# Optimization experiments

Hardware: AMD Instinct MI355X
Metric: run time of the kernel (lower is better)

Reference implementation:

```python
import jax, jax.numpy as jnp
import numpy as np

B, T, C, H, D = 16, 512, 464, 16, 29  # head_size = n_embd // n_head = 29
EPS = 1e-5


def setup_inputs() -> dict:
    key = jax.random.key(0)
    ks = jax.random.split(key, 8)
    x = jax.random.normal(ks[0], (B, T, C), dtype=jnp.float32)
    # relative-position indices: idx[i, j] = clip(i - j, 0, T-1)
    i = jnp.arange(T)
    pos_idx = jnp.clip(i[:, None] - i[None, :], 0, T - 1).astype(jnp.int64)
    s = 0.02
    wq = jax.random.normal(ks[1], (H, C, D), dtype=jnp.float32) * s
    wk = jax.random.normal(ks[2], (H, C, D), dtype=jnp.float32) * s
    wv = jax.random.normal(ks[3], (H, C, D), dtype=jnp.float32) * s
    pos_emb = jax.random.normal(ks[4], (H, T, 1), dtype=jnp.float32) * s
    w_proj = jax.random.normal(ks[5], (C, C), dtype=jnp.float32) * s
    b_proj = jnp.zeros((C,), dtype=jnp.float32)
    g1 = jnp.ones((C,), dtype=jnp.float32)
    g2 = jnp.ones((C,), dtype=jnp.float32)
    w1 = jax.random.normal(ks[6], (C, 4 * C), dtype=jnp.float32) * s
    w2 = jax.random.normal(ks[7], (4 * C, C), dtype=jnp.float32) * s
    return {"x": x, "pos_idx": pos_idx, "wq": wq, "wk": wk, "wv": wv,
            "pos_emb": pos_emb, "w_proj": w_proj, "b_proj": b_proj,
            "g1": g1, "g2": g2, "w1": w1, "w2": w2}


def _rmsnorm(x, g):
    return x * jax.lax.rsqrt(jnp.mean(x * x, axis=-1, keepdims=True) + EPS) * g


def reference(x, pos_idx, wq, wk, wv, pos_emb, w_proj, b_proj, g1, g2, w1, w2):
    t = x.shape[1]
    d = wq.shape[-1]
    scale = d ** -0.5
    h1 = _rmsnorm(x, g1)
    q = jnp.einsum('btc,hcd->bhtd', h1, wq)
    k = jnp.einsum('btc,hcd->bhtd', h1, wk)
    v = jnp.einsum('btc,hcd->bhtd', h1, wv)
    # per-head learned positional bias: (H, T, T), added BEFORE the 1/sqrt(d) scale
    bias = pos_emb[:, pos_idx[:t, :t], 0]
    attn = (jnp.einsum('bhtd,bhsd->bhts', q, k) + bias[None]) * scale
    causal = jnp.tril(jnp.ones((t, t), dtype=bool))
    attn = jnp.where(causal, attn, -jnp.inf)
    p = jax.nn.softmax(attn, axis=-1)
    o = jnp.einsum('bhts,bhsd->bhtd', p, v)
    o = o.transpose(0, 2, 1, 3).reshape(x.shape[0], t, -1)  # concat heads
    x = x + o @ w_proj + b_proj
    h2 = _rmsnorm(x, g2)
    x = x + jax.nn.silu(h2 @ w1) @ w2
    return x
```

## Files before the change

kernel.cpp:

```cpp
#include <hip/hip_runtime.h>
#include <math.h>

#define B_ 16
#define T_ 512
#define C_ 464
#define H_ 16
#define D_ 29
#define BT_ 8192
#define NQKV_P 1536
#define KP 480
#define C4 1856
#define C4P 1920
#define NPC 512

typedef __attribute__((ext_vector_type(8))) short short8;
typedef __attribute__((ext_vector_type(4))) float f32x4;
typedef __attribute__((ext_vector_type(16))) float f32x16;
typedef __attribute__((ext_vector_type(4))) unsigned short ushort4v;

static __device__ __forceinline__ unsigned short f2bf(float f) {
  union { float f; unsigned u; } v; v.f = f;
  unsigned r = v.u + 0x7FFFu + ((v.u >> 16) & 1u);
  return (unsigned short)(r >> 16);
}

static __device__ __forceinline__ void load_lds16(const void* g, void* l) {
  __builtin_amdgcn_global_load_lds((const __attribute__((address_space(1))) unsigned int*)g,
                                   (__attribute__((address_space(3))) unsigned int*)l,
                                   16, 0, 0);
}

#define CVTPK(dst, a, b) asm("v_cvt_pk_bf16_f32 %0, %1, %2" : "=v"(dst) : "v"(a), "v"(b))

#define PREP_BLOCKS 11152

__global__ void prep_norm(const float* __restrict__ wq, const float* __restrict__ wk,
                          const float* __restrict__ wv, const float* __restrict__ wproj,
                          const float* __restrict__ w1, const float* __restrict__ w2,
                          unsigned short* __restrict__ Wqkvt, unsigned short* __restrict__ Wprt,
                          unsigned short* __restrict__ W1t, unsigned short* __restrict__ W2t,
                          const float* __restrict__ X, const float* __restrict__ g1,
                          unsigned short* __restrict__ Y) {
  const int bid = blockIdx.x;
  if (bid < PREP_BLOCKS) {
    int idx = bid * 256 + threadIdx.x;
    const int S1 = NQKV_P * KP, S2 = NPC * KP, S3 = C4P * KP, S4 = NPC * C4;
    if (idx < S1) {
      int n = idx / KP, k = idx - n * KP;
      int which = n >> 9, h = (n >> 5) & 15, d = n & 31;
      float val = 0.f;
      if (d < D_ && k < C_) {
        const float* s = (which == 0) ? wq : (which == 1) ? wk : wv;
        val = s[((size_t)h * C_ + k) * D_ + d];
      }
      Wqkvt[idx] = f2bf(val);
      return;
    }
    idx -= S1;
    if (idx < S2) {
      int n = idx / KP, k = idx - n * KP;
      Wprt[idx] = f2bf((k < C_ && n < C_) ? wproj[(size_t)k * C_ + n] : 0.f);
      return;
    }
    idx -= S2;
    if (idx < S3) {
      int n = idx / KP, k = idx - n * KP;
      W1t[idx] = f2bf((k < C_ && n < C4) ? w1[(size_t)k * C4 + n] : 0.f);
      return;
    }
    idx -= S3;
    if (idx < S4) {
      int n = idx / C4, k = idx - n * C4;
      W2t[idx] = f2bf((n < C_) ? w2[(size_t)k * C_ + n] : 0.f);
    }
    return;
  }
  const int half = threadIdx.x >> 7;
  const int tid = threadIdx.x & 127;
  const int row = (bid - PREP_BLOCKS) * 2 + half;
  __shared__ float red[4];
  float4 v = make_float4(0.f, 0.f, 0.f, 0.f);
  float ss = 0.f;
  if (tid < C_ / 4) {
    v = ((const float4*)(X + (size_t)row * C_))[tid];
    ss = v.x * v.x + v.y * v.y + v.z * v.z + v.w * v.w;
  }
  #pragma unroll
  for (int off = 32; off > 0; off >>= 1) ss += __shfl_xor(ss, off);
  if ((threadIdx.x & 63) == 0) red[threadIdx.x >> 6] = ss;
  __syncthreads();
  float rs = rsqrtf((red[2 * half] + red[2 * half + 1]) * (1.f / C_) + 1e-5f);
  if (tid < C_ / 4) {
    float4 gg = ((const float4*)g1)[tid];
    ushort4v y;
    y.x = f2bf(v.x * rs * gg.x); y.y = f2bf(v.y * rs * gg.y);
    y.z = f2bf(v.z * rs * gg.z); y.w = f2bf(v.w * rs * gg.w);
    *(ushort4v*)(Y + (size_t)row * KP + tid * 4) = y;
  } else if (tid < 120) {
    ushort4v z = {0, 0, 0, 0};
    *(ushort4v*)(Y + (size_t)row * KP + tid * 4) = z;
  }
}

__launch_bounds__(128)
__global__ void rmsnorm_bf16(const float* __restrict__ X, const float* __restrict__ g,
                             unsigned short* __restrict__ Y) {
  const int row = blockIdx.x;
  const int tid = threadIdx.x;
  __shared__ float red[2];
  float4 v = make_float4(0.f, 0.f, 0.f, 0.f);
  float ss = 0.f;
  if (tid < C_ / 4) {
    v = ((const float4*)(X + (size_t)row * C_))[tid];
    ss = v.x * v.x + v.y * v.y + v.z * v.z + v.w * v.w;
  }
  #pragma unroll
  for (int off = 32; off > 0; off >>= 1) ss += __shfl_xor(ss, off);
  if ((tid & 63) == 0) red[tid >> 6] = ss;
  __syncthreads();
  float rs = rsqrtf((red[0] + red[1]) * (1.f / C_) + 1e-5f);
  if (tid < C_ / 4) {
    float4 gg = ((const float4*)g)[tid];
    ushort4v y;
    y.x = f2bf(v.x * rs * gg.x); y.y = f2bf(v.y * rs * gg.y);
    y.z = f2bf(v.z * rs * gg.z); y.w = f2bf(v.w * rs * gg.w);
    *(ushort4v*)(Y + (size_t)row * KP + tid * 4) = y;
  } else if (tid < 120) {
    ushort4v z = {0, 0, 0, 0};
    *(ushort4v*)(Y + (size_t)row * KP + tid * 4) = z;
  }
}

template<int EPI, int BM, int NT, int KT>
__launch_bounds__(256)
__global__ void gemm_mfma(const unsigned short* __restrict__ A,
                          const unsigned short* __restrict__ Bt,
                          float* __restrict__ Cf, unsigned short* __restrict__ Cb,
                          const float* __restrict__ res, const float* __restrict__ bias,
                          int N, int ldc,
                          unsigned short* __restrict__ Kb2, unsigned short* __restrict__ Vt2) {
  constexpr int MF = BM / 32;
  constexpr int NF = NT / 32;
  constexpr int CA = BM / 64;
  constexpr int CB = NT / 64;
  constexpr int DEPTH = (CA + CB == 2) ? 4 : 3;
  constexpr int nk = KT >> 5;
  __shared__ __align__(16) unsigned short As[DEPTH][BM * 32];
  __shared__ __align__(16) unsigned short Bs[DEPTH][NT * 32];
  const int tid = threadIdx.x;
  const int w = tid >> 6, lane = tid & 63;
  const int bm = blockIdx.x * BM, bn = blockIdx.y * NT;

  const int q = lane >> 2;
  const int g = (lane & 3) ^ ((lane >> 3) & 3);
  const unsigned short* gA = A + (size_t)(bm + w * CA * 16 + q) * KT + g * 8;
  const unsigned short* gB = Bt + (size_t)(bn + w * CB * 16 + q) * KT + g * 8;

  const int fr = lane & 15;
  const int hi4 = lane >> 4;
  const int gp = hi4 ^ ((lane >> 1) & 3);
  const int wr = (w >> 1) * (BM / 2), wc = (w & 1) * (NT / 2);
  int aoff[MF], boff[NF];
  #pragma unroll
  for (int m = 0; m < MF; ++m) aoff[m] = (wr + m * 16 + fr) * 32 + gp * 8;
  #pragma unroll
  for (int n = 0; n < NF; ++n) boff[n] = (wc + n * 16 + fr) * 32 + gp * 8;

  f32x4 acc[MF][NF];
  #pragma unroll
  for (int m = 0; m < MF; ++m)
    #pragma unroll
    for (int n = 0; n < NF; ++n) acc[m][n] = (f32x4){0.f, 0.f, 0.f, 0.f};

#define STAGE(BUF, KO) do { \
    _Pragma("unroll") for (int j = 0; j < CA; ++j) \
      load_lds16(gA + (size_t)(j * 16) * KT + (KO), &As[BUF][(w * CA + j) * 512]); \
    _Pragma("unroll") for (int j = 0; j < CB; ++j) \
      load_lds16(gB + (size_t)(j * 16) * KT + (KO), &Bs[BUF][(w * CB + j) * 512]); \
  } while (0)

#define COMPUTE(BUF) do { \
    short8 af[MF], bf[NF]; \
    _Pragma("unroll") for (int m = 0; m < MF; ++m) af[m] = *(const short8*)(&As[BUF][0] + aoff[m]); \
    _Pragma("unroll") for (int n = 0; n < NF; ++n) bf[n] = *(const short8*)(&Bs[BUF][0] + boff[n]); \
    _Pragma("unroll") for (int m = 0; m < MF; ++m) \
      _Pragma("unroll") for (int n = 0; n < NF; ++n) \
        acc[m][n] = __builtin_amdgcn_mfma_f32_16x16x32_bf16(af[m], bf[n], acc[m][n], 0, 0, 0); \
  } while (0)

  STAGE(0, 0);
  STAGE(1, 32);
  if constexpr (DEPTH == 4) STAGE(2, 64);
  #pragma unroll
  for (int t = 0; t < nk; ++t) {
    if constexpr (DEPTH == 3) {
      if (t + 1 < nk) {
        if constexpr (CA + CB == 3) asm volatile("s_waitcnt vmcnt(3)" ::: "memory");
        else                        asm volatile("s_waitcnt vmcnt(4)" ::: "memory");
      } else {
        asm volatile("s_waitcnt vmcnt(0)" ::: "memory");
      }
    } else {
      if (t + 2 < nk)      asm volatile("s_waitcnt vmcnt(4)" ::: "memory");
      else if (t + 1 < nk) asm volatile("s_waitcnt vmcnt(2)" ::: "memory");
      else                 asm volatile("s_waitcnt vmcnt(0)" ::: "memory");
    }
    asm volatile("s_waitcnt lgkmcnt(0)" ::: "memory");
    __builtin_amdgcn_s_barrier();
    __builtin_amdgcn_sched_barrier(0);
    if constexpr (DEPTH == 3) {
      if (t + 2 < nk) STAGE((t + 2) % 3, (t + 2) * 32);
    } else {
      if (t + 3 < nk) STAGE((t + 3) & 3, (t + 3) * 32);
    }
    COMPUTE(DEPTH == 3 ? (t % 3) : (t & 3));
  }
#undef STAGE
#undef COMPUTE

  const int crow0 = bm + wr + hi4 * 4;
  const int ccol0 = bn + wc + fr;
  #pragma unroll
  for (int n = 0; n < NF; ++n) {
    const int col = ccol0 + n * 16;
    if (col >= N) continue;
    #pragma unroll
    for (int m = 0; m < MF; ++m) {
      #pragma unroll
      for (int r = 0; r < 4; ++r) {
        const int row = crow0 + m * 16 + r;
        const size_t o = (size_t)row * ldc + col;
        float v = acc[m][n][r];
        if (EPI == 1) Cf[o] = res[o] + v + bias[col];
        else if (EPI == 2) Cb[o] = f2bf(v / (1.f + __expf(-v)));
        else if (EPI == 3) Cf[o] = res[o] + v;
        else if (EPI == 4) {
          int which = col >> 9;
          int hh = (col >> 5) & 15;
          int d = col & 31;
          unsigned short bv = f2bf(v);
          if (which < 2) {
            unsigned short* dst = (which == 0) ? Cb : Kb2;
            int pg = (d >> 3) ^ ((row >> 1) & 3);
            dst[(size_t)row * 512 + hh * 32 + pg * 8 + (d & 7)] = bv;
          } else {
            int tt = row & 511;
            int pg = ((tt >> 3) & 7) ^ (d & 7);
            Vt2[((size_t)(((row >> 9) * 16 + hh) * 32 + d)) * 512 + (tt & ~63) + pg * 8 + (tt & 7)] = bv;
          }
        }
      }
    }
  }
}

__launch_bounds__(128)
__global__ void attn_mfma(const unsigned short* __restrict__ Qb,
                          const unsigned short* __restrict__ Kb,
                          const unsigned short* __restrict__ Vt,
                          const float* __restrict__ pos_emb,
                          unsigned short* __restrict__ Ob) {
  __shared__ __align__(16) unsigned short Qs[2048];
  __shared__ __align__(16) unsigned short Ks[2][2048];
  __shared__ __align__(16) unsigned short Vs[2][2048];
  __shared__ __align__(16) float pes[512];
  const int blk = blockIdx.x;
  const int bh = blk & 255, qt = 7 - (blk >> 8);
  const int b = bh >> 4, h = bh & 15;
  const int tid = threadIdx.x;
  const int w = tid >> 6, lane = tid & 63;
  const int l31 = lane & 31, hi = lane >> 5;
  const int qb = qt * 64;

  const char* gq = (const char*)Qb + ((size_t)(b * 512 + qb) * 512 + h * 32) * 2;
  const char* gk = (const char*)Kb + ((size_t)(b * 512) * 512 + h * 32) * 2;
  const char* gv = (const char*)Vt + ((size_t)(bh * 32) * 512) * 2;

  #pragma unroll
  for (int j = 0; j < 2; ++j) {
    const int ci = (w * 2 + j) * 64 + lane;
    load_lds16(gq + (size_t)(ci >> 2) * 1024 + (lane & 3) * 16, (char*)Qs + (w * 2 + j) * 1024);
    load_lds16(gk + (size_t)(ci >> 2) * 1024 + (lane & 3) * 16, (char*)Ks[0] + (w * 2 + j) * 1024);
    load_lds16(gv + (size_t)(ci >> 3) * 1024 + (lane & 7) * 16, (char*)Vs[0] + (w * 2 + j) * 1024);
  }
  load_lds16((const char*)pos_emb + h * 2048 + tid * 16, (char*)pes + w * 1024);
  __syncthreads();

  const int qrow = w * 32 + l31;
  short8 qf[2];
  #pragma unroll
  for (int kc = 0; kc < 2; ++kc) {
    int pg = (hi + 2 * kc) ^ ((qrow >> 1) & 3);
    qf[kc] = *(const short8*)(Qs + qrow * 32 + pg * 8);
  }

  const int t = qb + w * 32 + l31;
  const int nt = qt + 1;
  const float scale2 = 0.18569533817705186f * 1.4426950408889634f;
  f32x16 oacc;
  #pragma unroll
  for (int r = 0; r < 16; ++r) oacc[r] = 0.f;
  float m_run = -1e30f, l_run = 0.f;

  for (int si = 0; si < nt; ++si) {
    const int c = si & 1;
    if (si + 1 < nt) {
      const int sb = (si + 1) * 64;
      #pragma unroll
      for (int j = 0; j < 2; ++j) {
        const int ci = (w * 2 + j) * 64 + lane;
        load_lds16(gk + (size_t)(sb + (ci >> 2)) * 1024 + (lane & 3) * 16,
                   (char*)Ks[c ^ 1] + (w * 2 + j) * 1024);
        load_lds16(gv + (size_t)(ci >> 3) * 1024 + sb * 2 + (lane & 7) * 16,
                   (char*)Vs[c ^ 1] + (w * 2 + j) * 1024);
      }
    }
    {
      const int sbase = si * 64;
      f32x16 sc[2];
      #pragma unroll
      for (int sf = 0; sf < 2; ++sf) {
        int srow = 32 * sf + l31;
        f32x16 a;
        #pragma unroll
        for (int r = 0; r < 16; ++r) a[r] = 0.f;
        #pragma unroll
        for (int kc = 0; kc < 2; ++kc) {
          int pg = (hi + 2 * kc) ^ ((srow >> 1) & 3);
          short8 kf = *(const short8*)(&Ks[c][0] + srow * 32 + pg * 8);
          a = __builtin_amdgcn_mfma_f32_32x32x16_bf16(kf, qf[kc], a, 0, 0, 0);
        }
        sc[sf] = a;
      }
      const bool edge = (si == nt - 1);
      float mt = -1e30f;
      #pragma unroll
      for (int sf = 0; sf < 2; ++sf)
        #pragma unroll
        for (int r = 0; r < 16; ++r) {
          int s_abs = sbase + 32 * sf + ((r & 3) + 8 * (r >> 2)) + 4 * hi;
          int idx = t - s_abs;
          float v;
          if (edge) {
            float bias = pes[idx < 0 ? 0 : idx];
            v = (sc[sf][r] + bias) * scale2;
            if (idx < 0) v = -1e30f;
          } else {
            v = (sc[sf][r] + pes[idx]) * scale2;
          }
          sc[sf][r] = v;
          mt = fmaxf(mt, v);
        }
      mt = fmaxf(mt, __shfl_xor(mt, 32));
      if (mt > m_run + 11.5f) {
        float corr = exp2f(m_run - mt);
        l_run *= corr;
        #pragma unroll
        for (int r = 0; r < 16; ++r) oacc[r] *= corr;
        m_run = mt;
      }
      float ls = 0.f;
      #pragma unroll
      for (int sf = 0; sf < 2; ++sf)
        #pragma unroll
        for (int r = 0; r < 16; ++r) {
          float p = exp2f(sc[sf][r] - m_run);
          sc[sf][r] = p;
          ls += p;
        }
      l_run += ls + __shfl_xor(ls, 32);
      unsigned pw[4][4];
      #pragma unroll
      for (int sf = 0; sf < 2; ++sf)
        #pragma unroll
        for (int kk = 0; kk < 2; ++kk) {
          const int kc = sf * 2 + kk;
          const int rb = kk * 8;
          unsigned pk01, pk23, pk45, pk67;
          CVTPK(pk01, sc[sf][rb + 0], sc[sf][rb + 1]);
          CVTPK(pk23, sc[sf][rb + 2], sc[sf][rb + 3]);
          CVTPK(pk45, sc[sf][rb + 4], sc[sf][rb + 5]);
          CVTPK(pk67, sc[sf][rb + 6], sc[sf][rb + 7]);
          asm volatile("v_permlane32_swap_b32 %0, %1" : "+v"(pk01), "+v"(pk45));
          asm volatile("v_permlane32_swap_b32 %0, %1" : "+v"(pk23), "+v"(pk67));
          pw[kc][0] = pk01; pw[kc][1] = pk23; pw[kc][2] = pk45; pw[kc][3] = pk67;
        }
      #pragma unroll
      for (int kc = 0; kc < 4; ++kc) {
        int pg = (2 * kc + hi) ^ (l31 & 7);
        short8 vf = *(const short8*)(&Vs[c][0] + l31 * 64 + pg * 8);
        union { unsigned u[4]; short8 s8; } pu;
        pu.u[0] = pw[kc][0]; pu.u[1] = pw[kc][1]; pu.u[2] = pw[kc][2]; pu.u[3] = pw[kc][3];
        oacc = __builtin_amdgcn_mfma_f32_32x32x16_bf16(vf, pu.s8, oacc, 0, 0, 0);
      }
    }
    __syncthreads();
  }

  const float inv = 1.f / l_run;
  #pragma unroll
  for (int r = 0; r < 16; ++r) {
    int d = (r & 3) + 8 * (r >> 2) + 4 * hi;
    if (d < D_)
      Ob[(size_t)(b * 512 + t) * KP + h * D_ + d] = f2bf(oacc[r] * inv);
  }
  if (h == 15 && tid < 64) {
    char* p = (char*)(Ob + (size_t)(b * 512 + qb + tid) * KP + C_);
    *(uint4*)p = make_uint4(0, 0, 0, 0);
    *(uint4*)(p + 16) = make_uint4(0, 0, 0, 0);
  }
}

extern "C" void kernel_launch(void* const* d_in, const int* in_sizes, int n_in,
                              void* d_out, int out_size, void* d_ws, size_t ws_size,
                              hipStream_t stream) {
  const float* x       = (const float*)d_in[0];
  const float* wq      = (const float*)d_in[2];
  const float* wk      = (const float*)d_in[3];
  const float* wv      = (const float*)d_in[4];
  const float* pos_emb = (const float*)d_in[5];
  const float* w_proj  = (const float*)d_in[6];
  const float* b_proj  = (const float*)d_in[7];
  const float* g1      = (const float*)d_in[8];
  const float* g2      = (const float*)d_in[9];
  const float* w1      = (const float*)d_in[10];
  const float* w2      = (const float*)d_in[11];
  float* out = (float*)d_out;

  char* cur = (char*)d_ws;
  auto alloc = [&](size_t bytes) { char* p = cur; cur += (bytes + 255) & ~(size_t)255; return p; };
  unsigned short* Wqkvt = (unsigned short*)alloc((size_t)NQKV_P * KP * 2);
  unsigned short* Wprt  = (unsigned short*)alloc((size_t)NPC * KP * 2);
  unsigned short* W1t   = (unsigned short*)alloc((size_t)C4P * KP * 2);
  unsigned short* W2t   = (unsigned short*)alloc((size_t)NPC * C4 * 2);
  unsigned short* h1b   = (unsigned short*)alloc((size_t)BT_ * KP * 2);
  unsigned short* ob    = (unsigned short*)alloc((size_t)BT_ * KP * 2);
  unsigned short* ffb   = (unsigned short*)alloc((size_t)BT_ * C4 * 2);
  unsigned short* Qbuf  = (unsigned short*)alloc((size_t)BT_ * 512 * 2);
  unsigned short* Kbuf  = (unsigned short*)alloc((size_t)BT_ * 512 * 2);
  unsigned short* Vtb   = (unsigned short*)alloc((size_t)BT_ * 512 * 2);

  prep_norm<<<PREP_BLOCKS + BT_ / 2, 256, 0, stream>>>(
      wq, wk, wv, w_proj, w1, w2, Wqkvt, Wprt, W1t, W2t, x, g1, h1b);

  gemm_mfma<4, 128, 64, KP><<<dim3(BT_ / 128, NQKV_P / 64), 256, 0, stream>>>(
      h1b, Wqkvt, nullptr, Qbuf, nullptr, nullptr, NQKV_P, 0, Kbuf, Vtb);
  attn_mfma<<<B_ * H_ * 8, 128, 0, stream>>>(Qbuf, Kbuf, Vtb, pos_emb, ob);
  gemm_mfma<1, 128, 64, KP><<<dim3(BT_ / 128, NPC / 64), 256, 0, stream>>>(
      ob, Wprt, out, nullptr, x, b_proj, C_, C_, nullptr, nullptr);
  rmsnorm_bf16<<<BT_, 128, 0, stream>>>(out, g2, h1b);
  gemm_mfma<2, 128, 64, KP><<<dim3(BT_ / 128, C4P / 64), 256, 0, stream>>>(
      h1b, W1t, nullptr, ffb, nullptr, nullptr, C4, C4, nullptr, nullptr);
  gemm_mfma<3, 128, 64, C4><<<dim3(BT_ / 128, NPC / 64), 256, 0, stream>>>(
      ffb, W2t, out, nullptr, out, nullptr, C_, C_, nullptr, nullptr);
}
```

Baseline: 160.0 us.

## Pad K to 512 and use 64-wide double-buffered K stages in GEMM

The GEMM main loop changes from a 3- or 4-deep pipeline of 32-wide K slices to a double buffer of 64-wide K slices. This halves the number of barrier and waitcnt rounds per tile, and each stage now issues two MFMA passes. The inner dimension padding grows from 480 to 512, so index math in weight prep becomes shifts and the row-padding stores widen. The W1 output padding from 1856 to 1920 is dropped, removing wasted tiles. In exchange, the K=464 GEMMs do more zero-padded MFMA work, and there is less prefetch depth, with loads issued only after compute finishes.

```diff
diff --git a/kernel.cpp b/kernel.cpp
--- a/kernel.cpp
+++ b/kernel.cpp
@@ -8,9 +8,8 @@
 #define D_ 29
 #define BT_ 8192
 #define NQKV_P 1536
-#define KP 480
+#define KP 512
 #define C4 1856
-#define C4P 1920
 #define NPC 512
 
 typedef __attribute__((ext_vector_type(8))) short short8;
@@ -32,7 +31,7 @@
 
 #define CVTPK(dst, a, b) asm("v_cvt_pk_bf16_f32 %0, %1, %2" : "=v"(dst) : "v"(a), "v"(b))
 
-#define PREP_BLOCKS 11152
+#define PREP_BLOCKS 11520
 
 __global__ void prep_norm(const float* __restrict__ wq, const float* __restrict__ wk,
                           const float* __restrict__ wv, const float* __restrict__ wproj,
@@ -44,9 +43,9 @@
   const int bid = blockIdx.x;
   if (bid < PREP_BLOCKS) {
     int idx = bid * 256 + threadIdx.x;
-    const int S1 = NQKV_P * KP, S2 = NPC * KP, S3 = C4P * KP, S4 = NPC * C4;
+    const int S1 = NQKV_P * KP, S2 = NPC * KP, S3 = C4 * KP, S4 = NPC * C4;
     if (idx < S1) {
-      int n = idx / KP, k = idx - n * KP;
+      int n = idx >> 9, k = idx & 511;
       int which = n >> 9, h = (n >> 5) & 15, d = n & 31;
       float val = 0.f;
       if (d < D_ && k < C_) {
@@ -58,14 +57,14 @@
     }
     idx -= S1;
     if (idx < S2) {
-      int n = idx / KP, k = idx - n * KP;
+      int n = idx >> 9, k = idx & 511;
       Wprt[idx] = f2bf((k < C_ && n < C_) ? wproj[(size_t)k * C_ + n] : 0.f);
       return;
     }
     idx -= S2;
     if (idx < S3) {
-      int n = idx / KP, k = idx - n * KP;
-      W1t[idx] = f2bf((k < C_ && n < C4) ? w1[(size_t)k * C4 + n] : 0.f);
+      int n = idx >> 9, k = idx & 511;
+      W1t[idx] = f2bf((k < C_) ? w1[(size_t)k * C4 + n] : 0.f);
       return;
     }
     idx -= S3;
@@ -96,7 +95,7 @@
     y.x = f2bf(v.x * rs * gg.x); y.y = f2bf(v.y * rs * gg.y);
     y.z = f2bf(v.z * rs * gg.z); y.w = f2bf(v.w * rs * gg.w);
     *(ushort4v*)(Y + (size_t)row * KP + tid * 4) = y;
-  } else if (tid < 120) {
+  } else {
     ushort4v z = {0, 0, 0, 0};
     *(ushort4v*)(Y + (size_t)row * KP + tid * 4) = z;
   }
@@ -125,7 +124,7 @@
     y.x = f2bf(v.x * rs * gg.x); y.y = f2bf(v.y * rs * gg.y);
     y.z = f2bf(v.z * rs * gg.z); y.w = f2bf(v.w * rs * gg.w);
     *(ushort4v*)(Y + (size_t)row * KP + tid * 4) = y;
-  } else if (tid < 120) {
+  } else {
     ushort4v z = {0, 0, 0, 0};
     *(ushort4v*)(Y + (size_t)row * KP + tid * 4) = z;
   }
@@ -143,10 +142,9 @@
   constexpr int NF = NT / 32;
   constexpr int CA = BM / 64;
   constexpr int CB = NT / 64;
-  constexpr int DEPTH = (CA + CB == 2) ? 4 : 3;
-  constexpr int nk = KT >> 5;
-  __shared__ __align__(16) unsigned short As[DEPTH][BM * 32];
-  __shared__ __align__(16) unsigned short Bs[DEPTH][NT * 32];
+  constexpr int nt = KT >> 6;
+  __shared__ __align__(16) unsigned short As[2][2 * BM * 32];
+  __shared__ __align__(16) unsigned short Bs[2][2 * NT * 32];
   const int tid = threadIdx.x;
   const int w = tid >> 6, lane = tid & 63;
   const int bm = blockIdx.x * BM, bn = blockIdx.y * NT;
@@ -172,51 +170,46 @@
     #pragma unroll
     for (int n = 0; n < NF; ++n) acc[m][n] = (f32x4){0.f, 0.f, 0.f, 0.f};
 
-#define STAGE(BUF, KO) do { \
+#define STAGE64(BUF, KO) do { \
     _Pragma("unroll") for (int j = 0; j < CA; ++j) \
       load_lds16(gA + (size_t)(j * 16) * KT + (KO), &As[BUF][(w * CA + j) * 512]); \
+    _Pragma("unroll") for (int j = 0; j < CA; ++j) \
+      load_lds16(gA + (size_t)(j * 16) * KT + (KO) + 32, &As[BUF][BM * 32 + (w * CA + j) * 512]); \
     _Pragma("unroll") for (int j = 0; j < CB; ++j) \
       load_lds16(gB + (size_t)(j * 16) * KT + (KO), &Bs[BUF][(w * CB + j) * 512]); \
+    _Pragma("unroll") for (int j = 0; j < CB; ++j) \
+      load_lds16(gB + (size_t)(j * 16) * KT + (KO) + 32, &Bs[BUF][NT * 32 + (w * CB + j) * 512]); \
   } while (0)
 
-#define COMPUTE(BUF) do { \
+#define COMPUTE32(BUF, HALF) do { \
     short8 af[MF], bf[NF]; \
-    _Pragma("unroll") for (int m = 0; m < MF; ++m) af[m] = *(const short8*)(&As[BUF][0] + aoff[m]); \
-    _Pragma("unroll") for (int n = 0; n < NF; ++n) bf[n] = *(const short8*)(&Bs[BUF][0] + boff[n]); \
+    _Pragma("unroll") for (int m = 0; m < MF; ++m) \
+      af[m] = *(const short8*)(&As[BUF][(HALF) * BM * 32] + aoff[m]); \
+    _Pragma("unroll") for (int n = 0; n < NF; ++n) \
+      bf[n] = *(const short8*)(&Bs[BUF][(HALF) * NT * 32] + boff[n]); \
     _Pragma("unroll") for (int m = 0; m < MF; ++m) \
       _Pragma("unroll") for (int n = 0; n < NF; ++n) \
         acc[m][n] = __builtin_amdgcn_mfma_f32_16x16x32_bf16(af[m], bf[n], acc[m][n], 0, 0, 0); \
   } while (0)
 
-  STAGE(0, 0);
-  STAGE(1, 32);
-  if constexpr (DEPTH == 4) STAGE(2, 64);
-  #pragma unroll
-  for (int t = 0; t < nk; ++t) {
-    if constexpr (DEPTH == 3) {
-      if (t + 1 < nk) {
-        if constexpr (CA + CB == 3) asm volatile("s_waitcnt vmcnt(3)" ::: "memory");
-        else                        asm volatile("s_waitcnt vmcnt(4)" ::: "memory");
-      } else {
-        asm volatile("s_waitcnt vmcnt(0)" ::: "memory");
-      }
-    } else {
-      if (t + 2 < nk)      asm volatile("s_waitcnt vmcnt(4)" ::: "memory");
-      else if (t + 1 < nk) asm volatile("s_waitcnt vmcnt(2)" ::: "memory");
-      else                 asm volatile("s_waitcnt vmcnt(0)" ::: "memory");
-    }
+  STAGE64(0, 0);
+  STAGE64(1, 64);
+  #pragma unroll
+  for (int t = 0; t < nt; ++t) {
+    if (t + 1 < nt) asm volatile("s_waitcnt vmcnt(6)" ::: "memory");
+    else            asm volatile("s_waitcnt vmcnt(0)" ::: "memory");
     asm volatile("s_waitcnt lgkmcnt(0)" ::: "memory");
     __builtin_amdgcn_s_barrier();
     __builtin_amdgcn_sched_barrier(0);
-    if constexpr (DEPTH == 3) {
-      if (t + 2 < nk) STAGE((t + 2) % 3, (t + 2) * 32);
-    } else {
-      if (t + 3 < nk) STAGE((t + 3) & 3, (t + 3) * 32);
-    }
-    COMPUTE(DEPTH == 3 ? (t % 3) : (t & 3));
-  }
-#undef STAGE
-#undef COMPUTE
+    COMPUTE32(t & 1, 0);
+    COMPUTE32(t & 1, 1);
+    asm volatile("s_waitcnt lgkmcnt(0)" ::: "memory");
+    __builtin_amdgcn_s_barrier();
+    __builtin_amdgcn_sched_barrier(0);
+    if (t + 2 < nt) STAGE64(t & 1, (t + 2) * 64);
+  }
+#undef STAGE64
+#undef COMPUTE32
 
   const int crow0 = bm + wr + hi4 * 4;
   const int ccol0 = bn + wc + fr;
@@ -408,6 +401,10 @@
     char* p = (char*)(Ob + (size_t)(b * 512 + qb + tid) * KP + C_);
     *(uint4*)p = make_uint4(0, 0, 0, 0);
     *(uint4*)(p + 16) = make_uint4(0, 0, 0, 0);
+    *(uint4*)(p + 32) = make_uint4(0, 0, 0, 0);
+    *(uint4*)(p + 48) = make_uint4(0, 0, 0, 0);
+    *(uint4*)(p + 64) = make_uint4(0, 0, 0, 0);
+    *(uint4*)(p + 80) = make_uint4(0, 0, 0, 0);
   }
 }
 
@@ -431,7 +428,7 @@
   auto alloc = [&](size_t bytes) { char* p = cur; cur += (bytes + 255) & ~(size_t)255; return p; };
   unsigned short* Wqkvt = (unsigned short*)alloc((size_t)NQKV_P * KP * 2);
   unsigned short* Wprt  = (unsigned short*)alloc((size_t)NPC * KP * 2);
-  unsigned short* W1t   = (unsigned short*)alloc((size_t)C4P * KP * 2);
+  unsigned short* W1t   = (unsigned short*)alloc((size_t)C4 * KP * 2);
   unsigned short* W2t   = (unsigned short*)alloc((size_t)NPC * C4 * 2);
   unsigned short* h1b   = (unsigned short*)alloc((size_t)BT_ * KP * 2);
   unsigned short* ob    = (unsigned short*)alloc((size_t)BT_ * KP * 2);
@@ -449,7 +446,7 @@
   gemm_mfma<1, 128, 64, KP><<<dim3(BT_ / 128, NPC / 64), 256, 0, stream>>>(
       ob, Wprt, out, nullptr, x, b_proj, C_, C_, nullptr, nullptr);
   rmsnorm_bf16<<<BT_, 128, 0, stream>>>(out, g2, h1b);
-  gemm_mfma<2, 128, 64, KP><<<dim3(BT_ / 128, C4P / 64), 256, 0, stream>>>(
+  gemm_mfma<2, 128, 64, KP><<<dim3(BT_ / 128, C4 / 64), 256, 0, stream>>>(
       h1b, W1t, nullptr, ffb, nullptr, nullptr, C4, C4, nullptr, nullptr);
   gemm_mfma<3, 128, 64, C4><<<dim3(BT_ / 128, NPC / 64), 256, 0, stream>>>(
       ffb, W2t, out, nullptr, out, nullptr, C_, C_, nullptr, nullptr);
```

After: 148.0 us. 7.5% less time.
